# Performance work log

Hardware: AMD Instinct MI355X
Metric: run time of the kernel (lower is better)

## Reference

```python
import jax, jax.numpy as jnp
import numpy as np

D = 512   # word_dim
H = 4     # heads
NEG = -1.0e9


def setup_inputs() -> dict:
    key = jax.random.key(0)
    ks = jax.random.split(key, 9)
    B, N, K = 4, 1024, 32
    neibor_embedding = jax.random.normal(ks[0], (B, N, K, D), dtype=jnp.float32)
    x = jax.random.normal(ks[1], (B, N, D), dtype=jnp.float32)
    mask = jax.random.randint(ks[2], (B, N, K), 0, 2, dtype=jnp.int32)
    s = 1.0 / np.sqrt(D)
    Wq = jax.random.normal(ks[3], (D, D), dtype=jnp.float32) * s
    bq = jax.random.normal(ks[4], (D,), dtype=jnp.float32) * s
    Wk = jax.random.normal(ks[5], (D, D), dtype=jnp.float32) * s
    bk = jax.random.normal(ks[6], (D,), dtype=jnp.float32) * s
    Wv = jax.random.normal(ks[7], (D, D), dtype=jnp.float32) * s
    bv = jax.random.normal(ks[8], (D,), dtype=jnp.float32) * s
    return {"neibor_embedding": neibor_embedding, "mask": mask, "x": x,
            "Wq": Wq, "bq": bq, "Wk": Wk, "bk": bk, "Wv": Wv, "bv": bv}


def reference(neibor_embedding, mask, x, Wq, bq, Wk, bk, Wv, bv):
    B, N, K, Dm = neibor_embedding.shape
    dh = Dm // H
    # torch Linear: y = x @ W.T + b
    q = x @ Wq.T + bq                        # [B, N, D]
    k = neibor_embedding @ Wk.T + bk         # [B, N, K, D]
    v = neibor_embedding @ Wv.T + bv         # [B, N, K, D]
    q = q.reshape(B, N, H, dh)
    k = k.reshape(B, N, K, H, dh)
    v = v.reshape(B, N, K, H, dh)
    # broadcast q*k sum over head_dim -> scores [B, N, H, K] (no 1/sqrt(d) scaling, per source)
    scores = jnp.einsum('bnhd,bnkhd->bnhk', q, k)
    m = (mask[:, :, None, :] == 0)           # [B, N, 1, K] broadcasts over heads
    scores = jnp.where(m, NEG, scores)
    attn = jax.nn.softmax(scores, axis=3)    # [B, N, H, K]
    vec = jnp.einsum('bnhk,bnkhd->bnhd', attn, v)  # [B, N, H, dh]
    return vec.reshape(B, N, Dm)
```

## Files before the change

kernel.cpp:

```cpp
#include <hip/hip_runtime.h>

#define DD   512
#define KK_N 32
#define HH   4
#define DH   128
#define BN_TOT 4096

typedef __bf16 bf16x8 __attribute__((ext_vector_type(8)));
typedef float  f32x4  __attribute__((ext_vector_type(4)));

__device__ __forceinline__ unsigned rne_bf16(float x) {
    unsigned u = __float_as_uint(x);
    return (u + 0x7fffu + ((u >> 16) & 1u)) >> 16;
}

__global__ __launch_bounds__(256)
void prep_wkT(const float* __restrict__ Wk, float* __restrict__ WkT)
{
    __shared__ float tile[32][DH + 1];
    const int h = blockIdx.y, o0 = blockIdx.x * 32, t = threadIdx.x;
#pragma unroll
    for (int r = 0; r < 16; r++) {
        int k = (t >> 5) + r * 8;
        tile[t & 31][k] = Wk[(long)(h * DH + k) * DD + o0 + (t & 31)];
    }
    __syncthreads();
#pragma unroll
    for (int r = 0; r < 16; r++) {
        int ol = (t >> 7) + r * 2;
        WkT[((long)h * DD + o0 + ol) * DH + (t & 127)] = tile[ol][t & 127];
    }
}

template<int BM, int BN>
__global__ __launch_bounds__(256)
void gemm_bf16x2(const float* __restrict__ A, int lda, long sA,
                 const float* __restrict__ B, int ldb, long sB,
                 float*       __restrict__ C, int ldc, long sC,
                 const float* __restrict__ bias, int sBias,
                 int Kd)
{
    constexpr int BK  = 64;
    constexpr int LDW = 2 * BK + 8;
    constexpr int A_LOADS = BM * BK / 1024;
    constexpr int B_LOADS = BN * BK / 1024;
    constexpr int WM = BM / 2, WN = BN / 2;
    constexpr int MI = WM / 16, NI = WN / 16;

    const int z = blockIdx.z;
    A += (long)z * sA;
    B += (long)z * sB;
    C += (long)z * sC;
    if (bias) bias += (long)z * sBias;

    __shared__ __align__(16) unsigned short As[BM * LDW];
    __shared__ __align__(16) unsigned short Bs[BN * LDW];

    const int t    = threadIdx.x;
    const int lane = t & 63;
    const int wave = t >> 6;
    const int wm   = wave >> 1, wn = wave & 1;
    const int rbase = blockIdx.y * BM;
    const int obase = blockIdx.x * BN;

    float4 areg[A_LOADS], breg[B_LOADS];
    auto loadAB = [&](int k0) {
#pragma unroll
        for (int i = 0; i < A_LOADS; i++) {
            int s = t + i * 256, k4 = s & 15, row = s >> 4;
            areg[i] = *(const float4*)&A[(long)(rbase + row) * lda + k0 + k4 * 4];
        }
#pragma unroll
        for (int i = 0; i < B_LOADS; i++) {
            int s = t + i * 256, k4 = s & 15, row = s >> 4;
            breg[i] = *(const float4*)&B[(long)(obase + row) * ldb + k0 + k4 * 4];
        }
    };
    auto cvt_store = [&](unsigned short* dst, float4 v, int row, int k4) {
        unsigned h0 = rne_bf16(v.x), h1 = rne_bf16(v.y);
        unsigned h2 = rne_bf16(v.z), h3 = rne_bf16(v.w);
        float l0 = v.x - __uint_as_float(h0 << 16);
        float l1 = v.y - __uint_as_float(h1 << 16);
        float l2 = v.z - __uint_as_float(h2 << 16);
        float l3 = v.w - __uint_as_float(h3 << 16);
        int off = row * LDW + (k4 >> 1) * 16 + (k4 & 1) * 4;
        uint2 hw = make_uint2(h0 | (h1 << 16), h2 | (h3 << 16));
        uint2 lw = make_uint2(rne_bf16(l0) | (rne_bf16(l1) << 16),
                              rne_bf16(l2) | (rne_bf16(l3) << 16));
        *(uint2*)&dst[off]     = hw;
        *(uint2*)&dst[off + 8] = lw;
    };

    f32x4 acc[MI][NI];
#pragma unroll
    for (int m = 0; m < MI; m++)
#pragma unroll
        for (int n = 0; n < NI; n++)
            acc[m][n] = (f32x4){0.f, 0.f, 0.f, 0.f};

    const int a_base = (wm * WM + (lane & 15)) * LDW + (lane >> 4) * 16;
    const int b_base = (wn * WN + (lane & 15)) * LDW + (lane >> 4) * 16;

    loadAB(0);
    for (int k0 = 0; k0 < Kd; k0 += BK) {
        __syncthreads();
#pragma unroll
        for (int i = 0; i < A_LOADS; i++) { int s = t + i * 256; cvt_store(As, areg[i], s >> 4, s & 15); }
#pragma unroll
        for (int i = 0; i < B_LOADS; i++) { int s = t + i * 256; cvt_store(Bs, breg[i], s >> 4, s & 15); }
        __syncthreads();
        if (k0 + BK < Kd) loadAB(k0 + BK);

#pragma unroll
        for (int ks = 0; ks < 2; ks++) {
            bf16x8 ah[MI], al[MI], bh[NI], bl[NI];
#pragma unroll
            for (int m = 0; m < MI; m++) {
                ah[m] = *(const bf16x8*)&As[a_base + m * 16 * LDW + ks * 64];
                al[m] = *(const bf16x8*)&As[a_base + m * 16 * LDW + ks * 64 + 8];
            }
#pragma unroll
            for (int n = 0; n < NI; n++) {
                bh[n] = *(const bf16x8*)&Bs[b_base + n * 16 * LDW + ks * 64];
                bl[n] = *(const bf16x8*)&Bs[b_base + n * 16 * LDW + ks * 64 + 8];
            }
#pragma unroll
            for (int m = 0; m < MI; m++)
#pragma unroll
                for (int n = 0; n < NI; n++)
                    acc[m][n] = __builtin_amdgcn_mfma_f32_16x16x32_bf16(ah[m], bh[n], acc[m][n], 0, 0, 0);
#pragma unroll
            for (int m = 0; m < MI; m++)
#pragma unroll
                for (int n = 0; n < NI; n++)
                    acc[m][n] = __builtin_amdgcn_mfma_f32_16x16x32_bf16(ah[m], bl[n], acc[m][n], 0, 0, 0);
#pragma unroll
            for (int m = 0; m < MI; m++)
#pragma unroll
                for (int n = 0; n < NI; n++)
                    acc[m][n] = __builtin_amdgcn_mfma_f32_16x16x32_bf16(al[m], bh[n], acc[m][n], 0, 0, 0);
        }
    }

#pragma unroll
    for (int n = 0; n < NI; n++) {
        int col = obase + wn * WN + n * 16 + (lane & 15);
        float bv_ = bias ? bias[col] : 0.f;
#pragma unroll
        for (int m = 0; m < MI; m++) {
            int row0 = rbase + wm * WM + m * 16 + (lane >> 4) * 4;
#pragma unroll
            for (int j = 0; j < 4; j++)
                C[(long)(row0 + j) * ldc + col] = acc[m][n][j] + bv_;
        }
    }
}

__global__ __launch_bounds__(256)
void attn_fused(const float* __restrict__ ne,
                const int*   __restrict__ mask,
                const float* __restrict__ q,
                const float* g,
                const float* __restrict__ bk,
                float* wne)
{
    const int bn   = blockIdx.x;
    const int t    = threadIdx.x;
    const int wave = t >> 6;
    const int lane = t & 63;

    __shared__ __align__(16) float ne_s[16][516];
    __shared__ __align__(16) float g_s[HH * DD];
    __shared__ float part[4][16][HH];
    __shared__ float p_s[HH][16];
    __shared__ float c_s[HH];
    __shared__ float m_s[HH], l_s[HH], alpha_s[HH];

    {
        const float4* gs = (const float4*)(g + (long)bn * (HH * DD));
        float4 v0 = gs[t];
        float4 v1 = gs[t + 256];
        *(float4*)&g_s[t * 4]         = v0;
        *(float4*)&g_s[(t + 256) * 4] = v1;
    }
    {
        float2 q2 = *(const float2*)&q[(long)bn * DD + wave * DH + lane * 2];
        float2 b2 = *(const float2*)&bk[wave * DH + lane * 2];
        float cp = q2.x * b2.x + q2.y * b2.y;
#pragma unroll
        for (int off = 32; off >= 1; off >>= 1)
            cp += __shfl_xor(cp, off, 64);
        if (lane == 0) c_s[wave] = cp;
    }
    if (t < HH) { m_s[t] = -__builtin_inff(); l_s[t] = 0.f; }

    float wacc[8] = {};
    const int h_own = t >> 6;
    const int d8    = (t & 63) * 8;
    const int kk    = t & 15;
    const int rep   = t >> 4;

    for (int ch = 0; ch < 2; ch++) {
        __syncthreads();
        {
            const float4* src = (const float4*)(ne + (long)bn * (KK_N * DD) + ch * (16 * DD));
#pragma unroll
            for (int i = 0; i < 8; i++) {
                int f = i * 256 + t;
                float4 v = src[f];
                *(float4*)&ne_s[f >> 7][(f & 127) * 4] = v;
            }
        }
        __syncthreads();
        {
            float acc[HH] = {};
#pragma unroll
            for (int i = 0; i < 8; i++) {
                float4 nv = *(const float4*)&ne_s[kk][rep * 32 + i * 4];
#pragma unroll
                for (int h = 0; h < HH; h++) {
                    float4 gv = *(const float4*)&g_s[h * DD + rep * 32 + i * 4];
                    acc[h] = fmaf(nv.x, gv.x, acc[h]);
                    acc[h] = fmaf(nv.y, gv.y, acc[h]);
                    acc[h] = fmaf(nv.z, gv.z, acc[h]);
                    acc[h] = fmaf(nv.w, gv.w, acc[h]);
                }
            }
#pragma unroll
            for (int h = 0; h < HH; h++) {
                acc[h] += __shfl_xor(acc[h], 16, 64);
                acc[h] += __shfl_xor(acc[h], 32, 64);
            }
            if ((t & 48) == 0) {
#pragma unroll
                for (int h = 0; h < HH; h++) part[wave][kk][h] = acc[h];
            }
        }
        __syncthreads();
        if (t < 64) {
            int k_i = t & 15, h = t >> 4;
            float s = part[0][k_i][h] + part[1][k_i][h] + part[2][k_i][h]
                    + part[3][k_i][h] + c_s[h];
            if (mask[(long)bn * KK_N + ch * 16 + k_i] == 0) s = -1.0e9f;
            float mx = s;
#pragma unroll
            for (int off = 8; off >= 1; off >>= 1)
                mx = fmaxf(mx, __shfl_xor(mx, off, 64));
            float m_old = m_s[h];
            float m_new = fmaxf(m_old, mx);
            float p = expf(s - m_new);
            float sm = p;
#pragma unroll
            for (int off = 8; off >= 1; off >>= 1)
                sm += __shfl_xor(sm, off, 64);
            p_s[h][k_i] = p;
            if (k_i == 0) {
                float alpha = expf(m_old - m_new);
                alpha_s[h] = alpha;
                l_s[h] = l_s[h] * alpha + sm;
                m_s[h] = m_new;
            }
        }
        __syncthreads();
        {
            float alpha = alpha_s[h_own];
#pragma unroll
            for (int j = 0; j < 8; j++) wacc[j] *= alpha;
#pragma unroll
            for (int k2 = 0; k2 < 16; k2++) {
                float pk = p_s[h_own][k2];
                float4 n0 = *(const float4*)&ne_s[k2][d8];
                float4 n1 = *(const float4*)&ne_s[k2][d8 + 4];
                wacc[0] = fmaf(pk, n0.x, wacc[0]);
                wacc[1] = fmaf(pk, n0.y, wacc[1]);
                wacc[2] = fmaf(pk, n0.z, wacc[2]);
                wacc[3] = fmaf(pk, n0.w, wacc[3]);
                wacc[4] = fmaf(pk, n1.x, wacc[4]);
                wacc[5] = fmaf(pk, n1.y, wacc[5]);
                wacc[6] = fmaf(pk, n1.z, wacc[6]);
                wacc[7] = fmaf(pk, n1.w, wacc[7]);
            }
        }
    }
    float rl = 1.0f / l_s[h_own];
    float4 o0 = make_float4(wacc[0] * rl, wacc[1] * rl, wacc[2] * rl, wacc[3] * rl);
    float4 o1 = make_float4(wacc[4] * rl, wacc[5] * rl, wacc[6] * rl, wacc[7] * rl);
    float* dst = wne + (long)bn * (HH * DD) + t * 8;
    *(float4*)&dst[0] = o0;
    *(float4*)&dst[4] = o1;
}

extern "C" void kernel_launch(void* const* d_in, const int* in_sizes, int n_in,
                              void* d_out, int out_size, void* d_ws, size_t ws_size,
                              hipStream_t stream) {
    (void)in_sizes; (void)n_in; (void)out_size; (void)ws_size;
    const float* ne  = (const float*)d_in[0];
    const int*   msk = (const int*)  d_in[1];
    const float* x   = (const float*)d_in[2];
    const float* Wq  = (const float*)d_in[3];
    const float* bq  = (const float*)d_in[4];
    const float* Wk  = (const float*)d_in[5];
    const float* bk  = (const float*)d_in[6];
    const float* Wv  = (const float*)d_in[7];
    const float* bv  = (const float*)d_in[8];
    float* out = (float*)d_out;

    float* q_ws = (float*)d_ws;
    float* g_ws = q_ws + (long)BN_TOT * DD;
    float* wkT  = g_ws + (long)BN_TOT * HH * DD;

    dim3 blk(256);
    prep_wkT<<<dim3(16, HH), blk, 0, stream>>>(Wk, wkT);
    gemm_bf16x2<64, 128><<<dim3(DD / 128, BN_TOT / 64, 1), blk, 0, stream>>>(
        x, DD, 0, Wq, DD, 0, q_ws, DD, 0, bq, 0, DD);
    gemm_bf16x2<64, 128><<<dim3(DD / 128, BN_TOT / 64, HH), blk, 0, stream>>>(
        q_ws, DD, DH, wkT, DH, (long)DD * DH, g_ws, HH * DD, DD, nullptr, 0, DH);
    attn_fused<<<dim3(BN_TOT), blk, 0, stream>>>(ne, msk, q_ws, g_ws, bk, g_ws);
    gemm_bf16x2<64, 128><<<dim3(1, BN_TOT / 64, HH), blk, 0, stream>>>(
        g_ws, HH * DD, DD, Wv, DD, (long)DH * DD, out, DD, DH, bv, DH, DD);
}
```

Baseline: 446.7 us.

## Pre-split GEMM operands into bf16 hi/lo planes once instead of per tile

Adds a conversion kernel that splits x, Wq and Wv into bf16 high/low planes ahead of time. Producer kernels (prep_wkT, the Q GEMM, attention) now emit split bf16 outputs directly, so each GEMM loads pre-split operands and stores them straight to LDS without in-loop conversion. This removes repeated fp32-to-bf16x2 conversion ALU work in the GEMM main loops and keeps global traffic for those operands at the same byte count. In exchange it adds an extra launch and workspace buffers, and the attention output layout changes to split d into two halves.

Measured after the change: 514.5 us. 15.2% more time.

```diff
diff --git a/kernel.cpp b/kernel.cpp
--- a/kernel.cpp
+++ b/kernel.cpp
@@ -8,14 +8,38 @@
 
 typedef __bf16 bf16x8 __attribute__((ext_vector_type(8)));
 typedef float  f32x4  __attribute__((ext_vector_type(4)));
+typedef unsigned short u16;
 
 __device__ __forceinline__ unsigned rne_bf16(float x) {
     unsigned u = __float_as_uint(x);
     return (u + 0x7fffu + ((u >> 16) & 1u)) >> 16;
 }
+__device__ __forceinline__ float bf16_f(unsigned h16) {
+    return __uint_as_float(h16 << 16);
+}
 
 __global__ __launch_bounds__(256)
-void prep_wkT(const float* __restrict__ Wk, float* __restrict__ WkT)
+void cvt3(const float4* __restrict__ s0, u16* __restrict__ h0, u16* __restrict__ l0, int n0,
+          const float4* __restrict__ s1, u16* __restrict__ h1, u16* __restrict__ l1, int n1,
+          const float4* __restrict__ s2, u16* __restrict__ h2, u16* __restrict__ l2, int n2)
+{
+    int i = blockIdx.x * 256 + threadIdx.x;
+    const float4* s; u16* ph; u16* pl;
+    if (i < n0)                { s = s0; ph = h0; pl = l0; }
+    else if (i < n0 + n1)      { i -= n0;      s = s1; ph = h1; pl = l1; }
+    else if (i < n0 + n1 + n2) { i -= n0 + n1; s = s2; ph = h2; pl = l2; }
+    else return;
+    float4 v = s[i];
+    unsigned a = rne_bf16(v.x), b = rne_bf16(v.y), c = rne_bf16(v.z), d = rne_bf16(v.w);
+    float lx = v.x - bf16_f(a), ly = v.y - bf16_f(b);
+    float lz = v.z - bf16_f(c), lw = v.w - bf16_f(d);
+    *(uint2*)&ph[(long)i * 4] = make_uint2(a | (b << 16), c | (d << 16));
+    *(uint2*)&pl[(long)i * 4] = make_uint2(rne_bf16(lx) | (rne_bf16(ly) << 16),
+                                           rne_bf16(lz) | (rne_bf16(lw) << 16));
+}
+
+__global__ __launch_bounds__(256)
+void prep_wkT(const float* __restrict__ Wk, u16* __restrict__ WkTh, u16* __restrict__ WkTl)
 {
     __shared__ float tile[32][DH + 1];
     const int h = blockIdx.y, o0 = blockIdx.x * 32, t = threadIdx.x;
@@ -28,33 +52,39 @@
 #pragma unroll
     for (int r = 0; r < 16; r++) {
         int ol = (t >> 7) + r * 2;
-        WkT[((long)h * DD + o0 + ol) * DH + (t & 127)] = tile[ol][t & 127];
+        int k  = t & 127;
+        float v = tile[ol][k];
+        unsigned hb = rne_bf16(v);
+        long o = ((long)h * DD + o0 + ol) * DH + k;
+        WkTh[o] = (u16)hb;
+        WkTl[o] = (u16)rne_bf16(v - bf16_f(hb));
     }
 }
 
 template<int BM, int BN>
 __global__ __launch_bounds__(256)
-void gemm_bf16x2(const float* __restrict__ A, int lda, long sA,
-                 const float* __restrict__ B, int ldb, long sB,
-                 float*       __restrict__ C, int ldc, long sC,
-                 const float* __restrict__ bias, int sBias,
-                 int Kd)
+void gemm_pre(const u16* __restrict__ Ah, const u16* __restrict__ Al, int lda, long sA,
+              const u16* __restrict__ Bh, const u16* __restrict__ Bl, int ldb, long sB,
+              float* __restrict__ Cf, int ldc, long sC,
+              u16* __restrict__ Ch, u16* __restrict__ Cl, int ldch, long sCh,
+              const float* __restrict__ bias, int sBias, int Kd)
 {
     constexpr int BK  = 64;
     constexpr int LDW = 2 * BK + 8;
-    constexpr int A_LOADS = BM * BK / 1024;
-    constexpr int B_LOADS = BN * BK / 1024;
+    constexpr int AL = BM / 32;
+    constexpr int BL = BN / 32;
     constexpr int WM = BM / 2, WN = BN / 2;
     constexpr int MI = WM / 16, NI = WN / 16;
 
     const int z = blockIdx.z;
-    A += (long)z * sA;
-    B += (long)z * sB;
-    C += (long)z * sC;
+    Ah += (long)z * sA;  Al += (long)z * sA;
+    Bh += (long)z * sB;  Bl += (long)z * sB;
+    if (Cf)   Cf += (long)z * sC;
+    if (Ch) { Ch += (long)z * sCh; Cl += (long)z * sCh; }
     if (bias) bias += (long)z * sBias;
 
-    __shared__ __align__(16) unsigned short As[BM * LDW];
-    __shared__ __align__(16) unsigned short Bs[BN * LDW];
+    __shared__ __align__(16) u16 As[BM * LDW];
+    __shared__ __align__(16) u16 Bs[BN * LDW];
 
     const int t    = threadIdx.x;
     const int lane = t & 63;
@@ -63,32 +93,22 @@
     const int rbase = blockIdx.y * BM;
     const int obase = blockIdx.x * BN;
 
-    float4 areg[A_LOADS], breg[B_LOADS];
+    uint4 avh[AL], avl[AL], bvh[BL], bvl[BL];
     auto loadAB = [&](int k0) {
 #pragma unroll
-        for (int i = 0; i < A_LOADS; i++) {
-            int s = t + i * 256, k4 = s & 15, row = s >> 4;
-            areg[i] = *(const float4*)&A[(long)(rbase + row) * lda + k0 + k4 * 4];
-        }
-#pragma unroll
-        for (int i = 0; i < B_LOADS; i++) {
-            int s = t + i * 256, k4 = s & 15, row = s >> 4;
-            breg[i] = *(const float4*)&B[(long)(obase + row) * ldb + k0 + k4 * 4];
-        }
-    };
-    auto cvt_store = [&](unsigned short* dst, float4 v, int row, int k4) {
-        unsigned h0 = rne_bf16(v.x), h1 = rne_bf16(v.y);
-        unsigned h2 = rne_bf16(v.z), h3 = rne_bf16(v.w);
-        float l0 = v.x - __uint_as_float(h0 << 16);
-        float l1 = v.y - __uint_as_float(h1 << 16);
-        float l2 = v.z - __uint_as_float(h2 << 16);
-        float l3 = v.w - __uint_as_float(h3 << 16);
-        int off = row * LDW + (k4 >> 1) * 16 + (k4 & 1) * 4;
-        uint2 hw = make_uint2(h0 | (h1 << 16), h2 | (h3 << 16));
-        uint2 lw = make_uint2(rne_bf16(l0) | (rne_bf16(l1) << 16),
-                              rne_bf16(l2) | (rne_bf16(l3) << 16));
-        *(uint2*)&dst[off]     = hw;
-        *(uint2*)&dst[off + 8] = lw;
+        for (int i = 0; i < AL; i++) {
+            int s = t + i * 256, kg = s & 7, row = s >> 3;
+            long off = (long)(rbase + row) * lda + k0 + kg * 8;
+            avh[i] = *(const uint4*)&Ah[off];
+            avl[i] = *(const uint4*)&Al[off];
+        }
+#pragma unroll
+        for (int i = 0; i < BL; i++) {
+            int s = t + i * 256, kg = s & 7, row = s >> 3;
+            long off = (long)(obase + row) * ldb + k0 + kg * 8;
+            bvh[i] = *(const uint4*)&Bh[off];
+            bvl[i] = *(const uint4*)&Bl[off];
+        }
     };
 
     f32x4 acc[MI][NI];
@@ -105,9 +125,19 @@
     for (int k0 = 0; k0 < Kd; k0 += BK) {
         __syncthreads();
 #pragma unroll
-        for (int i = 0; i < A_LOADS; i++) { int s = t + i * 256; cvt_store(As, areg[i], s >> 4, s & 15); }
-#pragma unroll
-        for (int i = 0; i < B_LOADS; i++) { int s = t + i * 256; cvt_store(Bs, breg[i], s >> 4, s & 15); }
+        for (int i = 0; i < AL; i++) {
+            int s = t + i * 256, kg = s & 7, row = s >> 3;
+            int off = row * LDW + kg * 16;
+            *(uint4*)&As[off]     = avh[i];
+            *(uint4*)&As[off + 8] = avl[i];
+        }
+#pragma unroll
+        for (int i = 0; i < BL; i++) {
+            int s = t + i * 256, kg = s & 7, row = s >> 3;
+            int off = row * LDW + kg * 16;
+            *(uint4*)&Bs[off]     = bvh[i];
+            *(uint4*)&Bs[off + 8] = bvl[i];
+        }
         __syncthreads();
         if (k0 + BK < Kd) loadAB(k0 + BK);
 
@@ -150,8 +180,16 @@
         for (int m = 0; m < MI; m++) {
             int row0 = rbase + wm * WM + m * 16 + (lane >> 4) * 4;
 #pragma unroll
-            for (int j = 0; j < 4; j++)
-                C[(long)(row0 + j) * ldc + col] = acc[m][n][j] + bv_;
+            for (int j = 0; j < 4; j++) {
+                float val = acc[m][n][j] + bv_;
+                if (Cf) Cf[(long)(row0 + j) * ldc + col] = val;
+                if (Ch) {
+                    unsigned hb = rne_bf16(val);
+                    long o = (long)(row0 + j) * ldch + col;
+                    Ch[o] = (u16)hb;
+                    Cl[o] = (u16)rne_bf16(val - bf16_f(hb));
+                }
+            }
         }
     }
 }
@@ -159,10 +197,12 @@
 __global__ __launch_bounds__(256)
 void attn_fused(const float* __restrict__ ne,
                 const int*   __restrict__ mask,
-                const float* __restrict__ q,
-                const float* g,
+                const u16*   __restrict__ qh,
+                const u16*   __restrict__ ql,
+                const float* __restrict__ g,
                 const float* __restrict__ bk,
-                float* wne)
+                u16* __restrict__ wh,
+                u16* __restrict__ wl)
 {
     const int bn   = blockIdx.x;
     const int t    = threadIdx.x;
@@ -184,9 +224,13 @@
         *(float4*)&g_s[(t + 256) * 4] = v1;
     }
     {
-        float2 q2 = *(const float2*)&q[(long)bn * DD + wave * DH + lane * 2];
+        long qoff = (long)bn * DD + wave * DH + lane * 2;
+        unsigned uh = *(const unsigned*)&qh[qoff];
+        unsigned ul = *(const unsigned*)&ql[qoff];
+        float qx = __uint_as_float(uh << 16) + __uint_as_float(ul << 16);
+        float qy = __uint_as_float(uh & 0xffff0000u) + __uint_as_float(ul & 0xffff0000u);
         float2 b2 = *(const float2*)&bk[wave * DH + lane * 2];
-        float cp = q2.x * b2.x + q2.y * b2.y;
+        float cp = qx * b2.x + qy * b2.y;
 #pragma unroll
         for (int off = 32; off >= 1; off >>= 1)
             cp += __shfl_xor(cp, off, 64);
@@ -196,7 +240,7 @@
 
     float wacc[8] = {};
     const int h_own = t >> 6;
-    const int d8    = (t & 63) * 8;
+    const int dlo   = (t & 63) * 4;
     const int kk    = t & 15;
     const int rep   = t >> 4;
 
@@ -269,8 +313,8 @@
 #pragma unroll
             for (int k2 = 0; k2 < 16; k2++) {
                 float pk = p_s[h_own][k2];
-                float4 n0 = *(const float4*)&ne_s[k2][d8];
-                float4 n1 = *(const float4*)&ne_s[k2][d8 + 4];
+                float4 n0 = *(const float4*)&ne_s[k2][dlo];
+                float4 n1 = *(const float4*)&ne_s[k2][256 + dlo];
                 wacc[0] = fmaf(pk, n0.x, wacc[0]);
                 wacc[1] = fmaf(pk, n0.y, wacc[1]);
                 wacc[2] = fmaf(pk, n0.z, wacc[2]);
@@ -283,11 +327,18 @@
         }
     }
     float rl = 1.0f / l_s[h_own];
-    float4 o0 = make_float4(wacc[0] * rl, wacc[1] * rl, wacc[2] * rl, wacc[3] * rl);
-    float4 o1 = make_float4(wacc[4] * rl, wacc[5] * rl, wacc[6] * rl, wacc[7] * rl);
-    float* dst = wne + (long)bn * (HH * DD) + t * 8;
-    *(float4*)&dst[0] = o0;
-    *(float4*)&dst[4] = o1;
+    long b0 = (long)bn * (HH * DD) + h_own * DD + dlo;
+    unsigned hw[8], lw[8];
+#pragma unroll
+    for (int j = 0; j < 8; j++) {
+        float val = wacc[j] * rl;
+        hw[j] = rne_bf16(val);
+        lw[j] = rne_bf16(val - bf16_f(hw[j]));
+    }
+    *(uint2*)&wh[b0]       = make_uint2(hw[0] | (hw[1] << 16), hw[2] | (hw[3] << 16));
+    *(uint2*)&wl[b0]       = make_uint2(lw[0] | (lw[1] << 16), lw[2] | (lw[3] << 16));
+    *(uint2*)&wh[b0 + 256] = make_uint2(hw[4] | (hw[5] << 16), hw[6] | (hw[7] << 16));
+    *(uint2*)&wl[b0 + 256] = make_uint2(lw[4] | (lw[5] << 16), lw[6] | (lw[7] << 16));
 }
 
 extern "C" void kernel_launch(void* const* d_in, const int* in_sizes, int n_in,
@@ -305,17 +356,40 @@
     const float* bv  = (const float*)d_in[8];
     float* out = (float*)d_out;
 
-    float* q_ws = (float*)d_ws;
-    float* g_ws = q_ws + (long)BN_TOT * DD;
-    float* wkT  = g_ws + (long)BN_TOT * HH * DD;
+    const long NQ = (long)BN_TOT * DD;
+    const long NW = (long)DD * DD;
+    const long NG = (long)BN_TOT * HH * DD;
+
+    char* ws = (char*)d_ws;
+    u16* xh   = (u16*)ws;              ws += NQ * 2;
+    u16* xl   = (u16*)ws;              ws += NQ * 2;
+    u16* wqh  = (u16*)ws;              ws += NW * 2;
+    u16* wql  = (u16*)ws;              ws += NW * 2;
+    u16* wvh  = (u16*)ws;              ws += NW * 2;
+    u16* wvl  = (u16*)ws;              ws += NW * 2;
+    u16* wkTh = (u16*)ws;              ws += NW * 2;
+    u16* wkTl = (u16*)ws;              ws += NW * 2;
+    u16* qh   = (u16*)ws;              ws += NQ * 2;
+    u16* ql   = (u16*)ws;              ws += NQ * 2;
+    u16* wneh = (u16*)ws;              ws += NG * 2;
+    u16* wnel = (u16*)ws;              ws += NG * 2;
+    float* g_ws = (float*)ws;
 
     dim3 blk(256);
-    prep_wkT<<<dim3(16, HH), blk, 0, stream>>>(Wk, wkT);
-    gemm_bf16x2<64, 128><<<dim3(DD / 128, BN_TOT / 64, 1), blk, 0, stream>>>(
-        x, DD, 0, Wq, DD, 0, q_ws, DD, 0, bq, 0, DD);
-    gemm_bf16x2<64, 128><<<dim3(DD / 128, BN_TOT / 64, HH), blk, 0, stream>>>(
-        q_ws, DD, DH, wkT, DH, (long)DD * DH, g_ws, HH * DD, DD, nullptr, 0, DH);
-    attn_fused<<<dim3(BN_TOT), blk, 0, stream>>>(ne, msk, q_ws, g_ws, bk, g_ws);
-    gemm_bf16x2<64, 128><<<dim3(1, BN_TOT / 64, HH), blk, 0, stream>>>(
-        g_ws, HH * DD, DD, Wv, DD, (long)DH * DD, out, DD, DH, bv, DH, DD);
-}
+    const int n4x = (int)(NQ / 4), n4w = (int)(NW / 4);
+    cvt3<<<dim3((n4x + 2 * n4w) / 256), blk, 0, stream>>>(
+        (const float4*)x,  xh,  xl,  n4x,
+        (const float4*)Wq, wqh, wql, n4w,
+        (const float4*)Wv, wvh, wvl, n4w);
+    prep_wkT<<<dim3(16, HH), blk, 0, stream>>>(Wk, wkTh, wkTl);
+    gemm_pre<64, 128><<<dim3(DD / 128, BN_TOT / 64, 1), blk, 0, stream>>>(
+        xh, xl, DD, 0, wqh, wql, DD, 0,
+        nullptr, 0, 0, qh, ql, DD, 0, bq, 0, DD);
+    gemm_pre<64, 128><<<dim3(DD / 128, BN_TOT / 64, HH), blk, 0, stream>>>(
+        qh, ql, DD, DH, wkTh, wkTl, DH, (long)DD * DH,
+        g_ws, HH * DD, DD, nullptr, nullptr, 0, 0, nullptr, 0, DH);
+    attn_fused<<<dim3(BN_TOT), blk, 0, stream>>>(ne, msk, qh, ql, g_ws, bk, wneh, wnel);
+    gemm_pre<64, 128><<<dim3(1, BN_TOT / 64, HH), blk, 0, stream>>>(
+        wneh, wnel, HH * DD, DD, wvh, wvl, DD, (long)DH * DD,
+        out, DD, DH, nullptr, nullptr, 0, 0, bv, DH, DD);
+}
```
